# Kernel optimization log

Measured on AMD Instinct MI355X. Metric: run time of the kernel, lower is better.

## Reference

```python
import jax, jax.numpy as jnp
import numpy as np

MEMORY_SIZE = 512
PATTERN_DIM = 256
NUM_WAVELENGTHS = 3
ATTENTION_FOCUS = 1.0
CORRELATION_THRESHOLD = 0.3
H_NOISE = 0.03  # noise scale for the holographic medium buffer


def setup_inputs() -> dict:
    key = jax.random.key(0)
    k1, k2, k3 = jax.random.split(key, 3)
    B, R = 32, 128  # batch, rows per stimulus (R * PATTERN_DIM flat features)
    stimulus = jax.random.normal(k1, (B, R * PATTERN_DIM), dtype=jnp.float32)
    H_real = jax.random.normal(k2, (MEMORY_SIZE, PATTERN_DIM, NUM_WAVELENGTHS), dtype=jnp.float32) * H_NOISE
    H_imag = jax.random.normal(k3, (MEMORY_SIZE, PATTERN_DIM, NUM_WAVELENGTHS), dtype=jnp.float32) * H_NOISE
    return {"stimulus": stimulus, "H_real": H_real, "H_imag": H_imag}


def reference(stimulus, H_real, H_imag):
    # Faithful 'retrieve' mode of HolographicAssociativeMemory, fully vectorized.
    B = stimulus.shape[0]
    q = stimulus.reshape(B, -1, PATTERN_DIM).astype(jnp.complex64)  # [B, R, P]
    qf = jnp.fft.fft2(q, axes=(-2, -1))                             # [B, R, P]
    R = qf.shape[1]

    # query_fft[b, mem_idx % R] for every memory slot -> gather rows
    rows = jnp.arange(MEMORY_SIZE) % R
    q_rows = qf[:, rows, :]                                         # [B, M, P]

    H = (H_real + 1j * H_imag).astype(jnp.complex64)                # [M, P, W]
    phases = jnp.linspace(0.0, 2.0 * np.pi, NUM_WAVELENGTHS).astype(jnp.float32)
    ref_beams = jnp.exp(1j * phases).astype(jnp.complex64)          # [W]

    # reconstruction = query_fft_row * stored_hologram * reference_beam
    recon = q_rows[:, :, :, None] * H[None, :, :, :] * ref_beams    # [B, M, P, W]
    # torch.fft.ifft2 on a (1, P) tensor == ifft along P (size-1 axis is identity)
    rec = jnp.fft.ifft(recon, axis=2)                               # [B, M, P, W]
    corr = jnp.abs(rec).mean(axis=2)                                # [B, M, W]
    avg_corr = corr.mean(axis=-1)                                   # [B, M]

    focused = avg_corr * jnp.float32(ATTENTION_FOCUS)
    retrieved = jnp.where(focused > jnp.float32(CORRELATION_THRESHOLD), focused, jnp.float32(0.0))
    return retrieved
```

## Files before the change

### kernel.cpp

```cpp
#include <hip/hip_runtime.h>
#include <math.h>


#define TWO_PI 6.28318530717958647692f
#define PI_F   3.14159265358979323846f

#if __has_builtin(__builtin_amdgcn_permlane16_swap)
#define USE_PL16 1
#else
#define USE_PL16 0
#endif
#if __has_builtin(__builtin_amdgcn_permlane32_swap)
#define USE_PL32 1
#else
#define USE_PL32 0
#endif

typedef float f2 __attribute__((ext_vector_type(2)));
typedef unsigned int uint2v __attribute__((ext_vector_type(2)));

__device__ inline f2 mkf2(float x, float y) { f2 r; r[0] = x; r[1] = y; return r; }
__device__ inline f2 conjf2(f2 a) { return mkf2(a[0], -a[1]); }

__device__ inline f2 cmul(f2 a, f2 b) {
    const f2 axx = __builtin_shufflevector(a, a, 0, 0);
    const f2 ayn = mkf2(-a[1], a[1]);
    const f2 byx = __builtin_shufflevector(b, b, 1, 0);
    return axx * b + ayn * byx;
}
__device__ inline f2 csq(f2 a) { return cmul(a, a); }
__device__ inline f2 ab2(f2 A, f2 v, f2 B, f2 o) {
    const f2 Axx = __builtin_shufflevector(A, A, 0, 0);
    const f2 Ayn = mkf2(-A[1], A[1]);
    const f2 Bxx = __builtin_shufflevector(B, B, 0, 0);
    const f2 Byn = mkf2(-B[1], B[1]);
    const f2 vyx = __builtin_shufflevector(v, v, 1, 0);
    const f2 oyx = __builtin_shufflevector(o, o, 1, 0);
    return Axx * v + Ayn * vyx + Bxx * o + Byn * oyx;
}
__device__ inline f2 cfma2(f2 S, f2 b, f2 a) {
    const f2 Sxx = __builtin_shufflevector(S, S, 0, 0);
    const f2 Syn = mkf2(-S[1], S[1]);
    const f2 byx = __builtin_shufflevector(b, b, 1, 0);
    return Sxx * b + (Syn * byx + a);
}
__device__ inline f2 shfl_xor_c(f2 v, int mask) {
    return mkf2(__shfl_xor(v[0], mask, 64), __shfl_xor(v[1], mask, 64));
}

#define DPP_XOR1 0xB1
#define DPP_XOR2 0x4E
template <int CTRL>
__device__ inline f2 dpp_quad(f2 v) {
    return mkf2(
        __int_as_float(__builtin_amdgcn_update_dpp(__float_as_int(v[0]), __float_as_int(v[0]),
                                                   CTRL, 0xF, 0xF, false)),
        __int_as_float(__builtin_amdgcn_update_dpp(__float_as_int(v[1]), __float_as_int(v[1]),
                                                   CTRL, 0xF, 0xF, false)));
}

#if USE_PL16
__device__ inline void swap16c(f2 v, f2& a, f2& b) {
    uint2v rx = __builtin_amdgcn_permlane16_swap(__float_as_uint(v[0]), __float_as_uint(v[0]), false, false);
    uint2v ry = __builtin_amdgcn_permlane16_swap(__float_as_uint(v[1]), __float_as_uint(v[1]), false, false);
    a = mkf2(__uint_as_float(rx[0]), __uint_as_float(ry[0]));
    b = mkf2(__uint_as_float(rx[1]), __uint_as_float(ry[1]));
}
#endif
#if USE_PL32
__device__ inline void swap32c(f2 v, f2& a, f2& b) {
    uint2v rx = __builtin_amdgcn_permlane32_swap(__float_as_uint(v[0]), __float_as_uint(v[0]), false, false);
    uint2v ry = __builtin_amdgcn_permlane32_swap(__float_as_uint(v[1]), __float_as_uint(v[1]), false, false);
    a = mkf2(__uint_as_float(rx[0]), __uint_as_float(ry[0]));
    b = mkf2(__uint_as_float(rx[1]), __uint_as_float(ry[1]));
}
#endif

__global__ __launch_bounds__(256) void k_cols(const float* __restrict__ x,
                                              f2* __restrict__ yc,
                                              const float* __restrict__ Hr,
                                              const float* __restrict__ Hi,
                                              f2* __restrict__ Ht) {
    if (blockIdx.x >= 256) {
        const int idx = (blockIdx.x - 256) * 256 + threadIdx.x;
        const int m = idx / 768;
        const int rem = idx - m * 768;
        const int w = rem >> 8;
        const int p = rem & 255;
        const int k = __brev((unsigned)p) >> 24;
        const int src = (m * 256 + k) * 3 + w;
        Ht[idx] = mkf2(Hr[src], Hi[src]);
        return;
    }

    __shared__ f2 sm[128][17];
    __shared__ f2 tw[64];
    const int tid = threadIdx.x;

    if (tid < 64) {
        float sn, cs;
        __sincosf(-TWO_PI * (float)tid * (1.0f / 128.0f), &sn, &cs);
        tw[tid] = mkf2(cs, sn);
    }

    const int b  = blockIdx.x >> 3;
    const int d0 = (blockIdx.x & 7) << 4;
    const int c  = tid & 15;
    const int r0 = tid >> 4;
    const int d  = d0 + c;
    const size_t xb = (size_t)b * 32768;

#pragma unroll
    for (int r = r0; r < 128; r += 16) {
        sm[r][c] = mkf2(x[xb + (size_t)r * 256 + d],
                        x[xb + (size_t)r * 256 + d + 128]);
    }
    __syncthreads();

#pragma unroll
    for (int st = 0; st < 7; ++st) {
        const int h = 64 >> st;
#pragma unroll
        for (int k = 0; k < 4; ++k) {
            const int idx = tid + (k << 8);
            const int cc  = idx & 15;
            const int j   = idx >> 4;
            const int pos = j & (h - 1);
            const int i0  = (j << 1) - pos;
            const int i1  = i0 + h;
            const f2 w  = tw[pos << st];
            const f2 a  = sm[i0][cc];
            const f2 bv = sm[i1][cc];
            sm[i0][cc] = a + bv;
            sm[i1][cc] = cmul(a - bv, w);
        }
        __syncthreads();
    }

#pragma unroll
    for (int s = r0; s < 128; s += 16) {
        const int f  = __brev((unsigned)s) >> 25;
        const int pf = (128 - f) & 127;
        const int ps = __brev((unsigned)pf) >> 25;
        const f2 Zf = sm[s][c];
        const f2 Zp = sm[ps][c];
        const f2 sum = mkf2((Zf[0] + Zp[0]) * 0.5f, (Zf[1] - Zp[1]) * 0.5f);
        const f2 dif = mkf2((Zf[0] - Zp[0]) * 0.5f, (Zf[1] + Zp[1]) * 0.5f);
        const f2 Yb  = mkf2(dif[1], -dif[0]);
        const size_t row = ((size_t)b * 128 + s) * 256;
        yc[row + d]       = sum;
        yc[row + d + 128] = Yb;
    }
}

__global__ __launch_bounds__(256) void k_recon(const f2* __restrict__ yc,
                                               const f2* __restrict__ Ht,
                                               float* __restrict__ out) {
    __shared__ f2 sh[256];
    const int lane = threadIdx.x & 63;
    const int wid  = threadIdx.x >> 6;
    const int b    = blockIdx.x >> 7;
    const int r    = blockIdx.x & 127;
    const int m    = r + (wid << 7);
    const int rs   = __brev((unsigned)r) >> 25;

    float sn, cs;
    __sincosf(PI_F * (float)lane * (1.0f / 128.0f), &sn, &cs);
    const f2 wi0 = mkf2(cs, sn);
    const f2 w64 = csq(wi0);
    const f2 S32 = csq(w64);
    const f2 S16 = csq(S32);
    const f2 b16 = csq(S16);
    const f2 b32 = csq(b16);
    const f2 b64 = csq(b32);
    const f2 one = mkf2(1.0f, 0.0f);
    const f2 A8 = (lane & 8) ? b16 : one, B8 = (lane & 8) ? one : b16;
    const f2 A4 = (lane & 4) ? b32 : one, B4 = (lane & 4) ? one : b32;
    const f2 A2 = (lane & 2) ? b64 : one, B2 = (lane & 2) ? one : b64;
    const f2 sg1 = (lane & 1) ? mkf2(-1.0f, -1.0f) : mkf2(1.0f, 1.0f);
    const f2 wi1 = mkf2(-wi0[1], wi0[0]);
#if !USE_PL16
    const f2 A16 = (lane & 16) ? S16 : one, B16 = (lane & 16) ? one : S16;
#endif
#if !USE_PL32
    const f2 A32 = (lane & 32) ? S32 : one, B32 = (lane & 32) ? one : S32;
#endif

    {
        const f2 gam    = conjf2(wi0);
        const f2 w128_0 = gam;
        const f2 w128_1 = mkf2(gam[1], -gam[0]);
        const f2 w64f = conjf2(w64);
        const f2 g4   = conjf2(S32);
        const f2 g8   = conjf2(S16);
        const f2 g16  = conjf2(b16);
        const f2 g32  = conjf2(b32);
        const f2 g64  = conjf2(b64);
#if USE_PL32
        const f2 P32 = (lane & 32) ? mkf2(-g4[0], -g4[1]) : one;
        const f2 Q32 = (lane & 32) ? g4 : one;
#else
        const f2 A32f = (lane & 32) ? g4 : one;
        const f2 B32f = (lane & 32) ? mkf2(-g4[0], -g4[1]) : one;
#endif
#if USE_PL16
        const f2 P16 = (lane & 16) ? mkf2(-g8[0], -g8[1]) : one;
        const f2 Q16 = (lane & 16) ? g8 : one;
#else
        const f2 A16f = (lane & 16) ? g8 : one;
        const f2 B16f = (lane & 16) ? mkf2(-g8[0], -g8[1]) : one;
#endif
        const f2 A8f = (lane & 8) ? g16 : one;
        const f2 B8f = (lane & 8) ? mkf2(-g16[0], -g16[1]) : one;
        const f2 A4f = (lane & 4) ? g32 : one;
        const f2 B4f = (lane & 4) ? mkf2(-g32[0], -g32[1]) : one;
        const f2 A2f = (lane & 2) ? g64 : one;
        const f2 B2f = (lane & 2) ? mkf2(-g64[0], -g64[1]) : one;

        const f2* xr = yc + ((size_t)(b * 128 + rs)) * 256;
        f2 v0 = xr[lane];
        f2 v1 = xr[64 + lane];
        f2 v2 = xr[128 + lane];
        f2 v3 = xr[192 + lane];

        { f2 a = v0; v0 = a + v2; v2 = cmul(a - v2, w128_0); }
        { f2 a = v1; v1 = a + v3; v3 = cmul(a - v3, w128_1); }
        { f2 a = v0; v0 = a + v1; v1 = cmul(a - v1, w64f); }
        { f2 a = v2; v2 = a + v3; v3 = cmul(a - v3, w64f); }

        f2 u = (wid == 0) ? v0 : (wid == 1) ? v1 : (wid == 2) ? v2 : v3;

        {
#if USE_PL32
            f2 a, bb; swap32c(u, a, bb);
            u = ab2(P32, a, Q32, bb);
#else
            const f2 o = shfl_xor_c(u, 32);
            u = ab2(A32f, u, B32f, o);
#endif
        }
        {
#if USE_PL16
            f2 a, bb; swap16c(u, a, bb);
            u = ab2(P16, a, Q16, bb);
#else
            const f2 o = shfl_xor_c(u, 16);
            u = ab2(A16f, u, B16f, o);
#endif
        }
        { const f2 o = shfl_xor_c(u, 8); u = ab2(A8f, u, B8f, o); }
        { const f2 o = shfl_xor_c(u, 4); u = ab2(A4f, u, B4f, o); }
        { const f2 o = dpp_quad<DPP_XOR2>(u); u = ab2(A2f, u, B2f, o); }
        { const f2 o = dpp_quad<DPP_XOR1>(u); u = sg1 * u + o; }

        sh[(wid << 6) + lane] = u;
    }
    __syncthreads();

    f2 qv[4];
#pragma unroll
    for (int j = 0; j < 4; ++j) qv[j] = sh[j * 64 + lane];

    const f2* hp = Ht + (size_t)m * 768;
    f2 v[3][4];
#pragma unroll
    for (int w = 0; w < 3; ++w)
#pragma unroll
        for (int j = 0; j < 4; ++j)
            v[w][j] = cmul(qv[j], hp[w * 256 + j * 64 + lane]);

#pragma unroll
    for (int w = 0; w < 3; ++w)
#pragma unroll
        for (int j = 0; j < 4; ++j) {
            const f2 o = dpp_quad<DPP_XOR1>(v[w][j]);
            v[w][j] = sg1 * v[w][j] + o;
        }
#pragma unroll
    for (int w = 0; w < 3; ++w)
#pragma unroll
        for (int j = 0; j < 4; ++j) {
            const f2 o = dpp_quad<DPP_XOR2>(v[w][j]);
            v[w][j] = ab2(A2, v[w][j], B2, o);
        }
#pragma unroll
    for (int w = 0; w < 3; ++w)
#pragma unroll
        for (int j = 0; j < 4; ++j) {
            const f2 o = shfl_xor_c(v[w][j], 4);
            v[w][j] = ab2(A4, v[w][j], B4, o);
        }
#pragma unroll
    for (int w = 0; w < 3; ++w)
#pragma unroll
        for (int j = 0; j < 4; ++j) {
            const f2 o = shfl_xor_c(v[w][j], 8);
            v[w][j] = ab2(A8, v[w][j], B8, o);
        }
#pragma unroll
    for (int w = 0; w < 3; ++w)
#pragma unroll
        for (int j = 0; j < 4; ++j) {
#if USE_PL16
            f2 a, bb; swap16c(v[w][j], a, bb);
            v[w][j] = cfma2(S16, bb, a);
#else
            const f2 o = shfl_xor_c(v[w][j], 16);
            v[w][j] = ab2(A16, v[w][j], B16, o);
#endif
        }
#pragma unroll
    for (int w = 0; w < 3; ++w)
#pragma unroll
        for (int j = 0; j < 4; ++j) {
#if USE_PL32
            f2 a, bb; swap32c(v[w][j], a, bb);
            v[w][j] = cfma2(S32, bb, a);
#else
            const f2 o = shfl_xor_c(v[w][j], 32);
            v[w][j] = ab2(A32, v[w][j], B32, o);
#endif
        }
#pragma unroll
    for (int w = 0; w < 3; ++w) {
        f2 tv = cmul(w64, v[w][1]);
        f2 a = v[w][0];
        v[w][0] = a + tv; v[w][1] = a - tv;
        tv = cmul(w64, v[w][3]);
        a = v[w][2];
        v[w][2] = a + tv; v[w][3] = a - tv;
        tv = cmul(wi0, v[w][2]);
        a = v[w][0];
        v[w][0] = a + tv; v[w][2] = a - tv;
        tv = cmul(wi1, v[w][3]);
        a = v[w][1];
        v[w][1] = a + tv; v[w][3] = a - tv;
    }

    float acc = 0.0f;
#pragma unroll
    for (int w = 0; w < 3; ++w)
#pragma unroll
        for (int j = 0; j < 4; ++j) {
            const f2 sq = v[w][j] * v[w][j];
            acc += __builtin_amdgcn_sqrtf(sq[0] + sq[1]);
        }

#pragma unroll
    for (int off = 32; off > 0; off >>= 1) acc += __shfl_xor(acc, off, 64);

    if (lane == 0) {
        const float focused = acc * (1.0f / (256.0f * 256.0f * 3.0f));
        out[b * 512 + m] = (focused > 0.3f) ? focused : 0.0f;
    }
}

extern "C" void kernel_launch(void* const* d_in, const int* in_sizes, int n_in,
                              void* d_out, int out_size, void* d_ws, size_t ws_size,
                              hipStream_t stream) {
    (void)in_sizes; (void)n_in; (void)out_size; (void)ws_size;
    const float* stim = (const float*)d_in[0];
    const float* Hr   = (const float*)d_in[1];
    const float* Hi   = (const float*)d_in[2];
    float* out = (float*)d_out;

    f2* yc = (f2*)d_ws;
    f2* Ht = (f2*)((char*)d_ws + (size_t)32 * 128 * 256 * sizeof(f2));

    k_cols<<<256 + 1536, 256, 0, stream>>>(stim, yc, Hr, Hi, Ht);
    k_recon<<<4096, 256, 0, stream>>>(yc, Ht, out);
}
```

Before: 38.72 us.

## Store intermediate spectra and transposed holograms in fp16 with coalesced hologram transpose

The column-FFT output and the reordered hologram buffer are now stored as half-precision complex pairs instead of fp32, halving workspace write and read traffic between the two kernels. The hologram reorder now uses one block per memory slot: it loads contiguously into shared memory, then writes out in bit-reversed order, so global reads are coalesced and fewer blocks are launched. All arithmetic stays in fp32 after conversion. The risk is precision loss, since fp16 rounding of the FFT intermediates and hologram values may shift correlations near the threshold.

```diff
diff --git a/kernel.cpp b/kernel.cpp
--- a/kernel.cpp
+++ b/kernel.cpp
@@ -17,10 +17,13 @@
 #endif
 
 typedef float f2 __attribute__((ext_vector_type(2)));
+typedef _Float16 h2v __attribute__((ext_vector_type(2)));
 typedef unsigned int uint2v __attribute__((ext_vector_type(2)));
 
 __device__ inline f2 mkf2(float x, float y) { f2 r; r[0] = x; r[1] = y; return r; }
 __device__ inline f2 conjf2(f2 a) { return mkf2(a[0], -a[1]); }
+__device__ inline h2v f2h(f2 v) { h2v h; h[0] = (_Float16)v[0]; h[1] = (_Float16)v[1]; return h; }
+__device__ inline f2 h2f(h2v h) { f2 r; r[0] = (float)h[0]; r[1] = (float)h[1]; return r; }
 
 __device__ inline f2 cmul(f2 a, f2 b) {
     const f2 axx = __builtin_shufflevector(a, a, 0, 0);
@@ -77,25 +80,35 @@
 #endif
 
 __global__ __launch_bounds__(256) void k_cols(const float* __restrict__ x,
-                                              f2* __restrict__ yc,
+                                              h2v* __restrict__ yh,
                                               const float* __restrict__ Hr,
                                               const float* __restrict__ Hi,
-                                              f2* __restrict__ Ht) {
+                                              h2v* __restrict__ Hth) {
+    const int tid = threadIdx.x;
+
     if (blockIdx.x >= 256) {
-        const int idx = (blockIdx.x - 256) * 256 + threadIdx.x;
-        const int m = idx / 768;
-        const int rem = idx - m * 768;
-        const int w = rem >> 8;
-        const int p = rem & 255;
-        const int k = __brev((unsigned)p) >> 24;
-        const int src = (m * 256 + k) * 3 + w;
-        Ht[idx] = mkf2(Hr[src], Hi[src]);
+        const int m = blockIdx.x - 256;
+        __shared__ h2v hl[768];
+        const float* hr = Hr + (size_t)m * 768;
+        const float* hi = Hi + (size_t)m * 768;
+#pragma unroll
+        for (int i = tid; i < 768; i += 256) {
+            hl[i] = f2h(mkf2(hr[i], hi[i]));
+        }
+        __syncthreads();
+        h2v* ho = Hth + (size_t)m * 768;
+#pragma unroll
+        for (int o = tid; o < 768; o += 256) {
+            const int w = o >> 8;
+            const int p = o & 255;
+            const int k = __brev((unsigned)p) >> 24;
+            ho[o] = hl[k * 3 + w];
+        }
         return;
     }
 
     __shared__ f2 sm[128][17];
     __shared__ f2 tw[64];
-    const int tid = threadIdx.x;
 
     if (tid < 64) {
         float sn, cs;
@@ -148,13 +161,13 @@
         const f2 dif = mkf2((Zf[0] - Zp[0]) * 0.5f, (Zf[1] + Zp[1]) * 0.5f);
         const f2 Yb  = mkf2(dif[1], -dif[0]);
         const size_t row = ((size_t)b * 128 + s) * 256;
-        yc[row + d]       = sum;
-        yc[row + d + 128] = Yb;
-    }
-}
-
-__global__ __launch_bounds__(256) void k_recon(const f2* __restrict__ yc,
-                                               const f2* __restrict__ Ht,
+        yh[row + d]       = f2h(sum);
+        yh[row + d + 128] = f2h(Yb);
+    }
+}
+
+__global__ __launch_bounds__(256) void k_recon(const h2v* __restrict__ yh,
+                                               const h2v* __restrict__ Hth,
                                                float* __restrict__ out) {
     __shared__ f2 sh[256];
     const int lane = threadIdx.x & 63;
@@ -217,11 +230,11 @@
         const f2 A2f = (lane & 2) ? g64 : one;
         const f2 B2f = (lane & 2) ? mkf2(-g64[0], -g64[1]) : one;
 
-        const f2* xr = yc + ((size_t)(b * 128 + rs)) * 256;
-        f2 v0 = xr[lane];
-        f2 v1 = xr[64 + lane];
-        f2 v2 = xr[128 + lane];
-        f2 v3 = xr[192 + lane];
+        const h2v* xr = yh + ((size_t)(b * 128 + rs)) * 256;
+        f2 v0 = h2f(xr[lane]);
+        f2 v1 = h2f(xr[64 + lane]);
+        f2 v2 = h2f(xr[128 + lane]);
+        f2 v3 = h2f(xr[192 + lane]);
 
         { f2 a = v0; v0 = a + v2; v2 = cmul(a - v2, w128_0); }
         { f2 a = v1; v1 = a + v3; v3 = cmul(a - v3, w128_1); }
@@ -261,13 +274,13 @@
 #pragma unroll
     for (int j = 0; j < 4; ++j) qv[j] = sh[j * 64 + lane];
 
-    const f2* hp = Ht + (size_t)m * 768;
+    const h2v* hp = Hth + (size_t)m * 768;
     f2 v[3][4];
 #pragma unroll
     for (int w = 0; w < 3; ++w)
 #pragma unroll
         for (int j = 0; j < 4; ++j)
-            v[w][j] = cmul(qv[j], hp[w * 256 + j * 64 + lane]);
+            v[w][j] = cmul(qv[j], h2f(hp[w * 256 + j * 64 + lane]));
 
 #pragma unroll
     for (int w = 0; w < 3; ++w)
@@ -364,9 +377,9 @@
     const float* Hi   = (const float*)d_in[2];
     float* out = (float*)d_out;
 
-    f2* yc = (f2*)d_ws;
-    f2* Ht = (f2*)((char*)d_ws + (size_t)32 * 128 * 256 * sizeof(f2));
-
-    k_cols<<<256 + 1536, 256, 0, stream>>>(stim, yc, Hr, Hi, Ht);
-    k_recon<<<4096, 256, 0, stream>>>(yc, Ht, out);
-}
+    h2v* yh  = (h2v*)d_ws;
+    h2v* Hth = (h2v*)((char*)d_ws + (size_t)32 * 128 * 256 * sizeof(h2v));
+
+    k_cols<<<256 + 512, 256, 0, stream>>>(stim, yh, Hr, Hi, Hth);
+    k_recon<<<4096, 256, 0, stream>>>(yh, Hth, out);
+}
```

New measurement: 35.37 us (median of 2 runs). 1.09x faster.
